# Optimization experiments

Measured on AMD Instinct MI355X. Metric: run time of the kernel, lower is better.

## Reference

```python
import jax, jax.numpy as jnp
import numpy as np

B, N, D, K, H, L = 4, 20000, 64, 256, 4, 2
F = 4 * D
DH = D // H
SCALE = DH ** -0.5
EPS = 1e-5


def _layernorm(x, g, b):
    m = jnp.mean(x, axis=-1, keepdims=True)
    v = jnp.mean(jnp.square(x - m), axis=-1, keepdims=True)
    return (x - m) / jnp.sqrt(v + EPS) * g + b


def setup_inputs() -> dict:
    key = jax.random.key(0)
    ks = jax.random.split(key, 12)
    s = 0.02
    return {
        'expr': jax.random.normal(ks[0], (B, N), jnp.float32),
        'emb': jax.random.normal(ks[1], (N, D), jnp.float32),
        'Wq': jax.random.normal(ks[2], (L, D, D), jnp.float32) * s,
        'Wk': jax.random.normal(ks[3], (L, D, D), jnp.float32) * s,
        'Wv': jax.random.normal(ks[4], (L, D, D), jnp.float32) * s,
        'projK': jax.random.normal(ks[5], (L, N, K), jnp.float32) * s,
        'projV': jax.random.normal(ks[6], (L, N, K), jnp.float32) * s,
        'Wo': jax.random.normal(ks[7], (L, D, D), jnp.float32) * s,
        'bo': jnp.zeros((L, D), jnp.float32),
        'g1': jnp.ones((L, D), jnp.float32),
        'be1': jnp.zeros((L, D), jnp.float32),
        'W1': jax.random.normal(ks[8], (L, D, F), jnp.float32) * s,
        'bf1': jnp.zeros((L, F), jnp.float32),
        'W2': jax.random.normal(ks[9], (L, F, D), jnp.float32) * s,
        'bf2': jnp.zeros((L, D), jnp.float32),
        'g2': jnp.ones((L, D), jnp.float32),
        'be2': jnp.zeros((L, D), jnp.float32),
    }


def _forward(expr, emb, Wq, Wk, Wv, projK, projV, Wo, bo, g1, be1, W1, bf1, W2, bf2, g2, be2):
    # gene_ids = arange(N) for every batch row -> embedding lookup is just the table
    x = emb[None, :, :] * expr[:, :, None]  # [B, N, D]
    for i in range(L):
        b = x.shape[0]
        # Linformer self-attention
        q = jnp.einsum('bnd,de->bne', x, Wq[i])                 # [B, N, D]
        k_low = jnp.einsum('bnd,nk->bkd', x, projK[i])          # [B, K, D]
        v_low = jnp.einsum('bnd,nk->bkd', x, projV[i])          # [B, K, D]
        k = jnp.einsum('bkd,de->bke', k_low, Wk[i])             # [B, K, D]
        v = jnp.einsum('bkd,de->bke', v_low, Wv[i])             # [B, K, D]
        qh = q.reshape(b, N, H, DH).transpose(0, 2, 1, 3)       # [B, H, N, DH]
        kh = k.reshape(b, K, H, DH).transpose(0, 2, 1, 3)       # [B, H, K, DH]
        vh = v.reshape(b, K, H, DH).transpose(0, 2, 1, 3)       # [B, H, K, DH]
        dots = jnp.einsum('bhnd,bhkd->bhnk', qh, kh) * SCALE    # [B, H, N, K]
        attn = jax.nn.softmax(dots, axis=-1)
        o = jnp.einsum('bhnk,bhkd->bhnd', attn, vh)             # [B, H, N, DH]
        o = o.transpose(0, 2, 1, 3).reshape(b, N, D)
        o = jnp.einsum('bnd,de->bne', o, Wo[i]) + bo[i]
        x = _layernorm(o + x, g1[i], be1[i])
        # FFN (exact GELU, matching torch nn.GELU default)
        h = jax.nn.gelu(jnp.einsum('bnd,df->bnf', x, W1[i]) + bf1[i], approximate=False)
        f = jnp.einsum('bnf,fd->bnd', h, W2[i]) + bf2[i]
        x = _layernorm(f + x, g2[i], be2[i])
    return x


def reference(expr, emb, Wq, Wk, Wv, projK, projV, Wo, bo, g1, be1, W1, bf1, W2, bf2, g2, be2):
    return _forward(expr, emb, Wq, Wk, Wv, projK, projV, Wo, bo, g1, be1, W1, bf1, W2, bf2, g2, be2)
```

## Files before the change

### kernel.cpp

```cpp
#include <hip/hip_runtime.h>

using u16 = unsigned short;
typedef __bf16 bf16x8 __attribute__((ext_vector_type(8)));
typedef u16    u16x8  __attribute__((ext_vector_type(8)));
typedef u16    u16x4  __attribute__((ext_vector_type(4)));
typedef float  f32x4  __attribute__((ext_vector_type(4)));
typedef float  f32x16 __attribute__((ext_vector_type(16)));
typedef unsigned uint4v __attribute__((ext_vector_type(4)));

#define DEV static __device__ __forceinline__

constexpr int NB = 4;
constexpr int NN = 20000;
constexpr int DD = 64;
constexpr int KK = 256;
constexpr int NT = 313;
constexpr int ROWS = NB * NN;

DEV float b2f(u16 u) { union { unsigned i; float f; } c; c.i = ((unsigned)u) << 16; return c.f; }
DEV u16 f2b(float f) {
  union { float f; unsigned i; } c; c.f = f;
  unsigned i = c.i + 0x7FFFu + ((c.i >> 16) & 1u);
  return (u16)(i >> 16);
}
DEV bf16x8 ldb8(const u16* p) { return *reinterpret_cast<const bf16x8*>(p); }
DEV f32x16 mfma32(bf16x8 a, bf16x8 b, f32x16 c) { return __builtin_amdgcn_mfma_f32_32x32x16_bf16(a, b, c, 0, 0, 0); }

DEV unsigned cvtpk(float lo, float hi) {
  unsigned r;
  asm("v_cvt_pk_bf16_f32 %0, %1, %2" : "=v"(r) : "v"(lo), "v"(hi));
  return r;
}
DEV void swap32(unsigned& a, unsigned& b) {
  auto r = __builtin_amdgcn_permlane32_swap((int)a, (int)b, false, false);
  a = (unsigned)r[0]; b = (unsigned)r[1];
}

__global__ __launch_bounds__(256) void k_pre(
    const float* __restrict__ expr, const float* __restrict__ emb,
    const float* __restrict__ Wq, const float* __restrict__ Wo,
    const float* __restrict__ W1, const float* __restrict__ W2,
    const float* __restrict__ projK, const float* __restrict__ projV,
    u16* __restrict__ wb, u16* __restrict__ pKT, u16* __restrict__ pVT,
    u16* __restrict__ xb, u16* __restrict__ ones) {
  __shared__ unsigned Lt[256][33];
  int bid = blockIdx.x;
  int t = threadIdx.x;
  if (bid < 1252) {
    int tile = bid % NT, z = bid / NT;
    int layer = z & 1, pv = z >> 1;
    const float* src = (pv ? projV : projK) + (size_t)layer * NN * KK;
    u16* dst = (pv ? pVT : pKT) + ((size_t)layer * NT + tile) * (256 * 64);
    int w = t >> 6, l = t & 63;
    int n0 = tile * 64;
    float4 v[16];
#pragma unroll
    for (int i = 0; i < 16; ++i) {
      int n = n0 + w * 16 + i;
      v[i] = (n < NN) ? reinterpret_cast<const float4*>(src)[(size_t)n * 64 + l]
                      : make_float4(0.f, 0.f, 0.f, 0.f);
    }
    int swz = ((l >> 1) & 7) << 2;
#pragma unroll
    for (int j = 0; j < 8; ++j) {
      int npx = (w * 8 + j) ^ swz;
#pragma unroll
      for (int c = 0; c < 4; ++c) {
        float a = (&v[2 * j].x)[c], b = (&v[2 * j + 1].x)[c];
        Lt[4 * l + c][npx] = cvtpk(a, b);
      }
    }
    __syncthreads();
    int q = t & 7, kk = t >> 3;
#pragma unroll
    for (int p = 0; p < 8; ++p) {
      int k = p * 32 + kk;
      int base = (q * 4) ^ (((k >> 3) & 7) << 2);
      uint4v o;
      o.x = Lt[k][base + 0]; o.y = Lt[k][base + 1];
      o.z = Lt[k][base + 2]; o.w = Lt[k][base + 3];
      *reinterpret_cast<uint4v*>(&dst[(size_t)k * 64 + q * 8]) = o;
    }
  } else if (bid < 3752) {
    int idx8 = ((bid - 1252) * 256 + t) * 8;
    int b = idx8 / (NN * DD);
    int rem = idx8 - b * (NN * DD);
    int n = rem >> 6, d = rem & 63;
    float4 e0 = *reinterpret_cast<const float4*>(&emb[(n << 6) + d]);
    float4 e1 = *reinterpret_cast<const float4*>(&emb[(n << 6) + d + 4]);
    float s = expr[b * NN + n];
    u16x8 o;
    o[0] = f2b(e0.x * s); o[1] = f2b(e0.y * s); o[2] = f2b(e0.z * s); o[3] = f2b(e0.w * s);
    o[4] = f2b(e1.x * s); o[5] = f2b(e1.y * s); o[6] = f2b(e1.z * s); o[7] = f2b(e1.w * s);
    *reinterpret_cast<u16x8*>(&xb[idx8]) = o;
  } else if (bid < 3816) {
    int b2 = bid - 3752;
    int bx = b2 & 7, m = (b2 >> 3) & 3, l = b2 >> 5;
    int slot = bx * 256 + t;
    u16x8 o;
    if (m <= 1) {
      if (slot >= 512) return;
      int s = slot >> 7, rem = slot & 127;
      int ct = rem >> 6, lane = rem & 63;
      int hi = lane >> 5, lo = lane & 31;
      const float* src = (m == 0 ? Wq : Wo) + l * 4096;
      u16* dst = wb + (m == 0 ? 0 : 8192) + l * 4096;
#pragma unroll
      for (int j = 0; j < 8; ++j) o[j] = f2b(src[(s * 16 + hi * 8 + j) * 64 + ct * 32 + lo]);
      *reinterpret_cast<u16x8*>(&dst[slot * 8]) = o;
    } else if (m == 2) {
      int ftile = slot >> 8, s = (slot >> 6) & 3, lane = slot & 63;
      int hi = lane >> 5, lo = lane & 31;
      const float* src = W1 + l * 16384;
      u16* dst = wb + 16384 + l * 16384;
#pragma unroll
      for (int j = 0; j < 8; ++j) o[j] = f2b(src[(s * 16 + hi * 8 + j) * 256 + ftile * 32 + lo]);
      *reinterpret_cast<u16x8*>(&dst[slot * 8]) = o;
    } else {
      int dtile = slot >> 10, s2 = (slot >> 6) & 15, lane = slot & 63;
      int hi = lane >> 5, lo = lane & 31;
      const float* src = W2 + l * 16384;
      u16* dst = wb + 49152 + l * 16384;
#pragma unroll
      for (int j = 0; j < 8; ++j) o[j] = f2b(src[(s2 * 16 + hi * 8 + j) * 64 + dtile * 32 + lo]);
      *reinterpret_cast<u16x8*>(&dst[slot * 8]) = o;
    }
  } else {
    ones[t] = 0x3F80;
  }
}

__global__ __launch_bounds__(256) void k_qxt(
    const u16* __restrict__ x, const u16* __restrict__ WB,
    u16* __restrict__ qb, u16* __restrict__ xT) {
  __shared__ u16 LX[64][67];
  int bid = blockIdx.x;
  int t = threadIdx.x;
  if (bid < 625) {
    int w = t >> 6, lane = t & 63;
    int lo = lane & 31, hi = lane >> 5;
    int unit = bid * 4 + w;
    bf16x8 wf[4][2];
#pragma unroll
    for (int s = 0; s < 4; ++s)
#pragma unroll
      for (int ct = 0; ct < 2; ++ct) wf[s][ct] = ldb8(&WB[((s * 2 + ct) * 64 + lane) * 8]);
    f32x16 acc[2] = {};
    int r0 = unit * 32;
#pragma unroll
    for (int s = 0; s < 4; ++s) {
      bf16x8 a = ldb8(&x[(size_t)(r0 + lo) * 64 + s * 16 + hi * 8]);
      acc[0] = mfma32(a, wf[s][0], acc[0]);
      acc[1] = mfma32(a, wf[s][1], acc[1]);
    }
#pragma unroll
    for (int reg = 0; reg < 16; ++reg) {
      int row = r0 + (reg & 3) + 8 * (reg >> 2) + 4 * hi;
      qb[(size_t)row * 64 + lo] = f2b(acc[0][reg]);
      qb[(size_t)row * 64 + 32 + lo] = f2b(acc[1][reg]);
    }
  } else {
    int v2 = bid - 625;
    int tile = v2 % NT, b = v2 / NT;
    const u16* xbp = x + (size_t)b * NN * 64;
    int n0 = tile * 64;
    int q = t & 7, rr = t >> 3;
    u16x8 h0 = {}, h1 = {};
    int na = n0 + rr, nb2 = n0 + 32 + rr;
    if (na < NN) h0 = *reinterpret_cast<const u16x8*>(&xbp[(size_t)na * 64 + q * 8]);
    if (nb2 < NN) h1 = *reinterpret_cast<const u16x8*>(&xbp[(size_t)nb2 * 64 + q * 8]);
#pragma unroll
    for (int c = 0; c < 8; ++c) {
      LX[q * 8 + c][rr] = h0[c];
      LX[q * 8 + c][32 + rr] = h1[c];
    }
    __syncthreads();
    u16* dstx = xT + ((size_t)b * NT + tile) * 4096;
#pragma unroll
    for (int p = 0; p < 2; ++p) {
      int d = p * 32 + rr;
      u16x8 o;
#pragma unroll
      for (int i = 0; i < 8; ++i) o[i] = LX[d][q * 8 + i];
      *reinterpret_cast<u16x8*>(&dstx[(size_t)d * 64 + q * 8]) = o;
    }
  }
}

__global__ __launch_bounds__(256) void k_proj(
    const u16* __restrict__ xT, const u16* __restrict__ pKT_l, const u16* __restrict__ pVT_l,
    float* __restrict__ part) {
  int c = blockIdx.x, b = blockIdx.y, proj = blockIdx.z;
  const u16* P = proj ? pVT_l : pKT_l;
  const u16* xtb = xT + (size_t)b * NT * 4096;
  int t = threadIdx.x, w = t >> 6, lane = t & 63;
  int lo = lane & 31, hi = lane >> 5;
  int d0 = (w & 1) * 32;
  int kbase = (w >> 1) * 128;
  int n0 = c * 512;
  int rem = NN - n0;
  int steps = (rem < 512 ? rem : 512) >> 4;
  int arow = (d0 + lo) * 64;
  f32x16 acc[4] = {};
  int s = 0;
  for (; s + 4 <= steps; s += 4) {
    int tile = (n0 + s * 16) >> 6;
    const u16* xa = xtb + (size_t)tile * 4096;
    const u16* Pa = P + (size_t)tile * 16384;
    bf16x8 a[4]; bf16x8 bv[4][4];
#pragma unroll
    for (int u = 0; u < 4; ++u) {
      int ni = u * 16 + hi * 8;
      a[u] = ldb8(&xa[arow + ni]);
#pragma unroll
      for (int g = 0; g < 4; ++g) bv[u][g] = ldb8(&Pa[(kbase + g * 32 + lo) * 64 + ni]);
    }
#pragma unroll
    for (int u = 0; u < 4; ++u)
#pragma unroll
      for (int g = 0; g < 4; ++g) acc[g] = mfma32(a[u], bv[u][g], acc[g]);
  }
  for (; s < steps; ++s) {
    int nb = n0 + s * 16;
    int tile = nb >> 6, ni = (nb & 63) + hi * 8;
    const u16* xa = xtb + (size_t)tile * 4096;
    const u16* Pa = P + (size_t)tile * 16384;
    bf16x8 a = ldb8(&xa[arow + ni]);
#pragma unroll
    for (int g = 0; g < 4; ++g) acc[g] = mfma32(a, ldb8(&Pa[(kbase + g * 32 + lo) * 64 + ni]), acc[g]);
  }
  float* dst = part + ((size_t)(proj * NB + b) * 40 + c) * (64 * 256);
#pragma unroll
  for (int g = 0; g < 4; ++g)
#pragma unroll
    for (int r = 0; r < 16; ++r) {
      int d = d0 + (r & 3) + 8 * (r >> 2) + 4 * hi;
      dst[d * 256 + kbase + g * 32 + lo] = acc[g][r];
    }
}

__global__ __launch_bounds__(256) void k_p2(
    const float* __restrict__ part, const float* __restrict__ Wk_l, const float* __restrict__ Wv_l,
    u16* __restrict__ kbuf, u16* __restrict__ vT) {
  int ks = blockIdx.x, b = blockIdx.y, proj = blockIdx.z;
  int k0 = ks * 8;
  const float* W = proj ? Wv_l : Wk_l;
  __shared__ float low[64][8];
  int t = threadIdx.x;
  const float* src = part + (size_t)(proj * NB + b) * 40 * (64 * 256);
#pragma unroll
  for (int i = 0; i < 2; ++i) {
    int idx = i * 256 + t;
    int e = idx >> 3, k = idx & 7;
    float s = 0.f;
    for (int cc = 0; cc < 40; ++cc) s += src[(size_t)cc * (64 * 256) + e * 256 + k0 + k];
    low[e][k] = s;
  }
  __syncthreads();
#pragma unroll
  for (int i = 0; i < 2; ++i) {
    int idx = i * 256 + t;
    int d = idx & 63, kk = idx >> 6;
    float a = 0.f;
#pragma unroll
    for (int e = 0; e < 64; ++e) a += low[e][kk] * W[e * 64 + d];
    if (proj == 0) {
      kbuf[((size_t)b * KK + k0 + kk) * 64 + d] = f2b(a * 0.3606737602222409f);
    } else {
      vT[((size_t)b * 64 + d) * KK + k0 + kk] = f2b(a);
    }
  }
}

__global__ __launch_bounds__(256) void k_attn(
    const u16* __restrict__ q, const u16* __restrict__ kbuf, const u16* __restrict__ vT,
    const u16* __restrict__ ones, u16* __restrict__ ao) {
  int t = threadIdx.x, h = t >> 6, lane = t & 63;
  int lo = lane & 31, hi = lane >> 5;
  int b = blockIdx.y;
  int n0 = blockIdx.x * 32;
  const u16* qb = q + (size_t)b * NN * 64;
  const u16* kb = kbuf + (size_t)b * KK * 64 + h * 16;
  const u16* vsrc = (lo < 16)
      ? vT + (size_t)b * 64 * KK + (size_t)(h * 16 + lo) * KK
      : ones;
  bf16x8 qf = ldb8(&qb[(size_t)(n0 + lo) * 64 + h * 16 + hi * 8]);
  f32x16 acc = {};
#pragma unroll
  for (int kt = 0; kt < 8; ++kt) {
    bf16x8 kf = ldb8(&kb[(size_t)(kt * 32 + lo) * 64 + hi * 8]);
    f32x16 z = {};
    f32x16 s = mfma32(kf, qf, z);
    float e[16];
#pragma unroll
    for (int r = 0; r < 16; ++r) e[r] = __builtin_amdgcn_exp2f(s[r]);
#pragma unroll
    for (int c = 0; c < 2; ++c) {
      unsigned Aw = cvtpk(e[c * 8 + 0], e[c * 8 + 1]);
      unsigned Bw = cvtpk(e[c * 8 + 2], e[c * 8 + 3]);
      unsigned Cw = cvtpk(e[c * 8 + 4], e[c * 8 + 5]);
      unsigned Dw = cvtpk(e[c * 8 + 6], e[c * 8 + 7]);
      swap32(Aw, Cw);
      swap32(Bw, Dw);
      uint4v pk; pk.x = Aw; pk.y = Bw; pk.z = Cw; pk.w = Dw;
      bf16x8 af = ldb8(&vsrc[kt * 32 + c * 16 + hi * 8]);
      acc = mfma32(af, __builtin_bit_cast(bf16x8, pk), acc);
    }
  }
  float inv = __builtin_amdgcn_rcpf(acc[8]);
  float o[8];
#pragma unroll
  for (int r = 0; r < 8; ++r) o[r] = acc[r] * inv;
  unsigned Aw = cvtpk(o[0], o[1]);
  unsigned Bw = cvtpk(o[2], o[3]);
  unsigned Cw = cvtpk(o[4], o[5]);
  unsigned Dw = cvtpk(o[6], o[7]);
  swap32(Aw, Cw);
  swap32(Bw, Dw);
  uint4v st; st.x = Aw; st.y = Bw; st.z = Cw; st.w = Dw;
  *reinterpret_cast<uint4v*>(&ao[(size_t)b * NN * 64 + (size_t)(n0 + lo) * 64 + h * 16 + hi * 8]) = st;
}

__global__ __launch_bounds__(256) void k_oln(
    const u16* __restrict__ A, const u16* __restrict__ WB,
    const float* __restrict__ bias, const u16* __restrict__ res,
    const float* __restrict__ g, const float* __restrict__ be, u16* __restrict__ out) {
  int t = threadIdx.x, w = t >> 6, lane = t & 63;
  int lo = lane & 31, hi = lane >> 5;
  int unit = blockIdx.x * 4 + w;
  bf16x8 wf[4][2];
#pragma unroll
  for (int s = 0; s < 4; ++s)
#pragma unroll
    for (int ct = 0; ct < 2; ++ct) wf[s][ct] = ldb8(&WB[((s * 2 + ct) * 64 + lane) * 8]);
  float bia[2], gg[2], bb[2];
#pragma unroll
  for (int ct = 0; ct < 2; ++ct) {
    bia[ct] = bias[ct * 32 + lo];
    gg[ct] = g[ct * 32 + lo];
    bb[ct] = be[ct * 32 + lo];
  }
  f32x16 acc[2] = {};
  int r0 = unit * 32;
#pragma unroll
  for (int s = 0; s < 4; ++s) {
    bf16x8 a = ldb8(&A[(size_t)(r0 + lo) * 64 + s * 16 + hi * 8]);
    acc[0] = mfma32(a, wf[s][0], acc[0]);
    acc[1] = mfma32(a, wf[s][1], acc[1]);
  }
#pragma unroll
  for (int reg = 0; reg < 16; ++reg) {
    int row = r0 + (reg & 3) + 8 * (reg >> 2) + 4 * hi;
    float a0 = acc[0][reg] + bia[0] + b2f(res[(size_t)row * 64 + lo]);
    float a1 = acc[1][reg] + bia[1] + b2f(res[(size_t)row * 64 + 32 + lo]);
    float su = a0 + a1, sq = a0 * a0 + a1 * a1;
#pragma unroll
    for (int m = 1; m <= 16; m <<= 1) { su += __shfl_xor(su, m); sq += __shfl_xor(sq, m); }
    float mean = su * (1.f / 64.f);
    float var = sq * (1.f / 64.f) - mean * mean;
    float rstd = rsqrtf(var + 1e-5f);
    out[(size_t)row * 64 + lo] = f2b((a0 - mean) * rstd * gg[0] + bb[0]);
    out[(size_t)row * 64 + 32 + lo] = f2b((a1 - mean) * rstd * gg[1] + bb[1]);
  }
}

__global__ __launch_bounds__(256) void k_ffn(
    const u16* __restrict__ A, const u16* __restrict__ W1T, const u16* __restrict__ W2T,
    const float* __restrict__ b1, const float* __restrict__ b2,
    const float* __restrict__ g, const float* __restrict__ be,
    u16* __restrict__ outb, float* __restrict__ outf) {
  int t = threadIdx.x, w = t >> 6, lane = t & 63;
  int lo = lane & 31, hi = lane >> 5;
  int unit = blockIdx.x * 4 + w;
  int r0 = unit * 32;
  bf16x8 xf[4];
#pragma unroll
  for (int s = 0; s < 4; ++s) xf[s] = ldb8(&A[(size_t)(r0 + lo) * 64 + s * 16 + hi * 8]);
  f32x16 oacc[2] = {};
#pragma unroll
  for (int ft = 0; ft < 8; ++ft) {
    f32x16 hacc = {};
#pragma unroll
    for (int s = 0; s < 4; ++s)
      hacc = mfma32(ldb8(&W1T[((ft * 4 + s) * 64 + lane) * 8]), xf[s], hacc);
    float4 bb[4];
#pragma unroll
    for (int g4 = 0; g4 < 4; ++g4)
      bb[g4] = *reinterpret_cast<const float4*>(&b1[ft * 32 + g4 * 8 + 4 * hi]);
    float e[16];
#pragma unroll
    for (int r = 0; r < 16; ++r) {
      float z = hacc[r] + bb[r >> 2][r & 3];
      e[r] = 0.5f * z * (1.f + erff(z * 0.7071067811865475f));
    }
#pragma unroll
    for (int c = 0; c < 2; ++c) {
      unsigned Aw = cvtpk(e[c * 8 + 0], e[c * 8 + 1]);
      unsigned Bw = cvtpk(e[c * 8 + 2], e[c * 8 + 3]);
      unsigned Cw = cvtpk(e[c * 8 + 4], e[c * 8 + 5]);
      unsigned Dw = cvtpk(e[c * 8 + 6], e[c * 8 + 7]);
      swap32(Aw, Cw);
      swap32(Bw, Dw);
      uint4v pk; pk.x = Aw; pk.y = Bw; pk.z = Cw; pk.w = Dw;
      bf16x8 pf = __builtin_bit_cast(bf16x8, pk);
#pragma unroll
      for (int dt = 0; dt < 2; ++dt)
        oacc[dt] = mfma32(ldb8(&W2T[((dt * 16 + ft * 2 + c) * 64 + lane) * 8]), pf, oacc[dt]);
    }
  }
  int n = r0 + lo;
  float su = 0.f, sq = 0.f;
#pragma unroll
  for (int dt = 0; dt < 2; ++dt) {
#pragma unroll
    for (int m4 = 0; m4 < 4; ++m4) {
      int d0 = dt * 32 + m4 * 8 + 4 * hi;
      u16x4 rv = *reinterpret_cast<const u16x4*>(&A[(size_t)n * 64 + d0]);
      float4 b2v = *reinterpret_cast<const float4*>(&b2[d0]);
#pragma unroll
      for (int j = 0; j < 4; ++j) {
        int r = m4 * 4 + j;
        float val = oacc[dt][r] + b2v[j] + b2f(rv[j]);
        oacc[dt][r] = val;
        su += val; sq += val * val;
      }
    }
  }
  su += __shfl_xor(su, 32);
  sq += __shfl_xor(sq, 32);
  float mean = su * (1.f / 64.f);
  float var = sq * (1.f / 64.f) - mean * mean;
  float rstd = rsqrtf(var + 1e-5f);
#pragma unroll
  for (int dt = 0; dt < 2; ++dt) {
#pragma unroll
    for (int m4 = 0; m4 < 4; ++m4) {
      int d0 = dt * 32 + m4 * 8 + 4 * hi;
      float4 gv = *reinterpret_cast<const float4*>(&g[d0]);
      float4 bv = *reinterpret_cast<const float4*>(&be[d0]);
      float q0 = (oacc[dt][m4 * 4 + 0] - mean) * rstd * gv.x + bv.x;
      float q1 = (oacc[dt][m4 * 4 + 1] - mean) * rstd * gv.y + bv.y;
      float q2 = (oacc[dt][m4 * 4 + 2] - mean) * rstd * gv.z + bv.z;
      float q3 = (oacc[dt][m4 * 4 + 3] - mean) * rstd * gv.w + bv.w;
      if (outb) {
        unsigned w0 = cvtpk(q0, q1), w1 = cvtpk(q2, q3);
        u16x4 st = __builtin_bit_cast(u16x4, make_uint2(w0, w1));
        *reinterpret_cast<u16x4*>(&outb[(size_t)n * 64 + d0]) = st;
      }
      if (outf) {
        *reinterpret_cast<float4*>(&outf[(size_t)n * 64 + d0]) = make_float4(q0, q1, q2, q3);
      }
    }
  }
}

extern "C" void kernel_launch(void* const* d_in, const int* in_sizes, int n_in,
                              void* d_out, int out_size, void* d_ws, size_t ws_size,
                              hipStream_t stream) {
  const float* expr = (const float*)d_in[0];
  const float* emb  = (const float*)d_in[1];
  const float* Wq   = (const float*)d_in[2];
  const float* Wk   = (const float*)d_in[3];
  const float* Wv   = (const float*)d_in[4];
  const float* projK = (const float*)d_in[5];
  const float* projV = (const float*)d_in[6];
  const float* Wo   = (const float*)d_in[7];
  const float* bo   = (const float*)d_in[8];
  const float* g1   = (const float*)d_in[9];
  const float* be1  = (const float*)d_in[10];
  const float* W1   = (const float*)d_in[11];
  const float* bf1  = (const float*)d_in[12];
  const float* W2   = (const float*)d_in[13];
  const float* bf2  = (const float*)d_in[14];
  const float* g2   = (const float*)d_in[15];
  const float* be2  = (const float*)d_in[16];
  float* out = (float*)d_out;
  char* ws = (char*)d_ws;

  u16* xb0 = (u16*)(ws + 0);
  u16* xb1 = (u16*)(ws + 10240000);
  u16* xb2 = (u16*)(ws + 20480000);
  u16* qb  = (u16*)(ws + 30720000);
  u16* aob = (u16*)(ws + 40960000);
  float* part = (float*)(ws + 51200000);
  u16* pKT = (u16*)(ws + 72171520);
  u16* pVT = (u16*)(ws + 92684288);
  u16* xTb = (u16*)(ws + 113197056);
  u16* kB  = (u16*)(ws + 123453440);
  u16* vTB = (u16*)(ws + 123584512);
  u16* wb  = (u16*)(ws + 123715584);
  u16* ones = (u16*)(ws + 123879424);

  k_pre<<<3817, 256, 0, stream>>>(expr, emb, Wq, Wo, W1, W2, projK, projV,
                                  wb, pKT, pVT, xb0, ones);

  const size_t PL = (size_t)NT * 256 * 64;
  const u16* xin = xb0;
  for (int l = 0; l < 2; ++l) {
    const u16* wbq = wb + l * 4096;
    const u16* wbo = wb + 8192 + l * 4096;
    const u16* wb1 = wb + 16384 + l * 16384;
    const u16* wb2 = wb + 49152 + l * 16384;
    k_qxt<<<1877, 256, 0, stream>>>(xin, wbq, qb, xTb);
    k_proj<<<dim3(40, NB, 2), 256, 0, stream>>>(xTb, pKT + (size_t)l * PL, pVT + (size_t)l * PL, part);
    k_p2<<<dim3(32, NB, 2), 256, 0, stream>>>(part, Wk + l * 4096, Wv + l * 4096, kB, vTB);
    k_attn<<<dim3(625, NB), 256, 0, stream>>>(qb, kB, vTB, ones, aob);
    k_oln<<<625, 256, 0, stream>>>(aob, wbo, bo + l * 64, xin, g1 + l * 64, be1 + l * 64, xb1);
    k_ffn<<<625, 256, 0, stream>>>(xb1, wb1, wb2, bf1 + l * 256, bf2 + l * 64,
                                   g2 + l * 64, be2 + l * 64,
                                   l == 0 ? xb2 : nullptr, l == 1 ? out : nullptr);
    xin = xb2;
  }
}
```

Baseline: 422.6 us.

## Split projection grid over K halves and move Q projection into reduce kernel

The k_proj grid is doubled by splitting the K dimension into two halves, so each wave keeps two accumulators instead of four and the inner loop is unrolled eight steps deep. This raises block count from 320 to 640 to fill more compute units. The Q projection moves out of the transpose kernel and into k_p2, so the small reduction blocks run alongside the Q GEMM blocks instead of launching a nearly empty grid. The cost is reloading the x tile once per K half in k_proj.

New measurement: 415.8 us. No clear change (-1.6%).

```diff
diff --git a/kernel.cpp b/kernel.cpp
--- a/kernel.cpp
+++ b/kernel.cpp
@@ -130,95 +130,68 @@
   }
 }
 
-__global__ __launch_bounds__(256) void k_qxt(
-    const u16* __restrict__ x, const u16* __restrict__ WB,
-    u16* __restrict__ qb, u16* __restrict__ xT) {
+__global__ __launch_bounds__(256) void k_xt(const u16* __restrict__ x, u16* __restrict__ xT) {
   __shared__ u16 LX[64][67];
-  int bid = blockIdx.x;
+  int tile = blockIdx.x, b = blockIdx.y;
   int t = threadIdx.x;
-  if (bid < 625) {
-    int w = t >> 6, lane = t & 63;
-    int lo = lane & 31, hi = lane >> 5;
-    int unit = bid * 4 + w;
-    bf16x8 wf[4][2];
-#pragma unroll
-    for (int s = 0; s < 4; ++s)
-#pragma unroll
-      for (int ct = 0; ct < 2; ++ct) wf[s][ct] = ldb8(&WB[((s * 2 + ct) * 64 + lane) * 8]);
-    f32x16 acc[2] = {};
-    int r0 = unit * 32;
-#pragma unroll
-    for (int s = 0; s < 4; ++s) {
-      bf16x8 a = ldb8(&x[(size_t)(r0 + lo) * 64 + s * 16 + hi * 8]);
-      acc[0] = mfma32(a, wf[s][0], acc[0]);
-      acc[1] = mfma32(a, wf[s][1], acc[1]);
-    }
-#pragma unroll
-    for (int reg = 0; reg < 16; ++reg) {
-      int row = r0 + (reg & 3) + 8 * (reg >> 2) + 4 * hi;
-      qb[(size_t)row * 64 + lo] = f2b(acc[0][reg]);
-      qb[(size_t)row * 64 + 32 + lo] = f2b(acc[1][reg]);
-    }
-  } else {
-    int v2 = bid - 625;
-    int tile = v2 % NT, b = v2 / NT;
-    const u16* xbp = x + (size_t)b * NN * 64;
-    int n0 = tile * 64;
-    int q = t & 7, rr = t >> 3;
-    u16x8 h0 = {}, h1 = {};
-    int na = n0 + rr, nb2 = n0 + 32 + rr;
-    if (na < NN) h0 = *reinterpret_cast<const u16x8*>(&xbp[(size_t)na * 64 + q * 8]);
-    if (nb2 < NN) h1 = *reinterpret_cast<const u16x8*>(&xbp[(size_t)nb2 * 64 + q * 8]);
-#pragma unroll
-    for (int c = 0; c < 8; ++c) {
-      LX[q * 8 + c][rr] = h0[c];
-      LX[q * 8 + c][32 + rr] = h1[c];
-    }
-    __syncthreads();
-    u16* dstx = xT + ((size_t)b * NT + tile) * 4096;
-#pragma unroll
-    for (int p = 0; p < 2; ++p) {
-      int d = p * 32 + rr;
-      u16x8 o;
-#pragma unroll
-      for (int i = 0; i < 8; ++i) o[i] = LX[d][q * 8 + i];
-      *reinterpret_cast<u16x8*>(&dstx[(size_t)d * 64 + q * 8]) = o;
-    }
+  const u16* xbp = x + (size_t)b * NN * 64;
+  int n0 = tile * 64;
+  int q = t & 7, rr = t >> 3;
+  u16x8 h0 = {}, h1 = {};
+  int na = n0 + rr, nb2 = n0 + 32 + rr;
+  if (na < NN) h0 = *reinterpret_cast<const u16x8*>(&xbp[(size_t)na * 64 + q * 8]);
+  if (nb2 < NN) h1 = *reinterpret_cast<const u16x8*>(&xbp[(size_t)nb2 * 64 + q * 8]);
+#pragma unroll
+  for (int c = 0; c < 8; ++c) {
+    LX[q * 8 + c][rr] = h0[c];
+    LX[q * 8 + c][32 + rr] = h1[c];
+  }
+  __syncthreads();
+  u16* dstx = xT + ((size_t)b * NT + tile) * 4096;
+#pragma unroll
+  for (int p = 0; p < 2; ++p) {
+    int d = p * 32 + rr;
+    u16x8 o;
+#pragma unroll
+    for (int i = 0; i < 8; ++i) o[i] = LX[d][q * 8 + i];
+    *reinterpret_cast<u16x8*>(&dstx[(size_t)d * 64 + q * 8]) = o;
   }
 }
 
 __global__ __launch_bounds__(256) void k_proj(
     const u16* __restrict__ xT, const u16* __restrict__ pKT_l, const u16* __restrict__ pVT_l,
     float* __restrict__ part) {
-  int c = blockIdx.x, b = blockIdx.y, proj = blockIdx.z;
+  int c = blockIdx.x, b = blockIdx.y;
+  int proj = blockIdx.z & 1, ks = blockIdx.z >> 1;
   const u16* P = proj ? pVT_l : pKT_l;
   const u16* xtb = xT + (size_t)b * NT * 4096;
   int t = threadIdx.x, w = t >> 6, lane = t & 63;
   int lo = lane & 31, hi = lane >> 5;
   int d0 = (w & 1) * 32;
-  int kbase = (w >> 1) * 128;
+  int kbase = ks * 128 + (w >> 1) * 64;
   int n0 = c * 512;
   int rem = NN - n0;
   int steps = (rem < 512 ? rem : 512) >> 4;
   int arow = (d0 + lo) * 64;
-  f32x16 acc[4] = {};
+  f32x16 acc[2] = {};
   int s = 0;
-  for (; s + 4 <= steps; s += 4) {
-    int tile = (n0 + s * 16) >> 6;
-    const u16* xa = xtb + (size_t)tile * 4096;
-    const u16* Pa = P + (size_t)tile * 16384;
-    bf16x8 a[4]; bf16x8 bv[4][4];
-#pragma unroll
-    for (int u = 0; u < 4; ++u) {
-      int ni = u * 16 + hi * 8;
+  for (; s + 8 <= steps; s += 8) {
+    bf16x8 a[8]; bf16x8 bv[8][2];
+#pragma unroll
+    for (int u = 0; u < 8; ++u) {
+      int nb = n0 + (s + u) * 16;
+      int tile = nb >> 6, ni = (nb & 63) + hi * 8;
+      const u16* xa = xtb + (size_t)tile * 4096;
+      const u16* Pa = P + (size_t)tile * 16384;
       a[u] = ldb8(&xa[arow + ni]);
-#pragma unroll
-      for (int g = 0; g < 4; ++g) bv[u][g] = ldb8(&Pa[(kbase + g * 32 + lo) * 64 + ni]);
-    }
-#pragma unroll
-    for (int u = 0; u < 4; ++u)
-#pragma unroll
-      for (int g = 0; g < 4; ++g) acc[g] = mfma32(a[u], bv[u][g], acc[g]);
+      bv[u][0] = ldb8(&Pa[(kbase + lo) * 64 + ni]);
+      bv[u][1] = ldb8(&Pa[(kbase + 32 + lo) * 64 + ni]);
+    }
+#pragma unroll
+    for (int u = 0; u < 8; ++u) {
+      acc[0] = mfma32(a[u], bv[u][0], acc[0]);
+      acc[1] = mfma32(a[u], bv[u][1], acc[1]);
+    }
   }
   for (; s < steps; ++s) {
     int nb = n0 + s * 16;
@@ -226,12 +199,12 @@
     const u16* xa = xtb + (size_t)tile * 4096;
     const u16* Pa = P + (size_t)tile * 16384;
     bf16x8 a = ldb8(&xa[arow + ni]);
-#pragma unroll
-    for (int g = 0; g < 4; ++g) acc[g] = mfma32(a, ldb8(&Pa[(kbase + g * 32 + lo) * 64 + ni]), acc[g]);
+    acc[0] = mfma32(a, ldb8(&Pa[(kbase + lo) * 64 + ni]), acc[0]);
+    acc[1] = mfma32(a, ldb8(&Pa[(kbase + 32 + lo) * 64 + ni]), acc[1]);
   }
   float* dst = part + ((size_t)(proj * NB + b) * 40 + c) * (64 * 256);
 #pragma unroll
-  for (int g = 0; g < 4; ++g)
+  for (int g = 0; g < 2; ++g)
 #pragma unroll
     for (int r = 0; r < 16; ++r) {
       int d = d0 + (r & 3) + 8 * (r >> 2) + 4 * hi;
@@ -241,33 +214,60 @@
 
 __global__ __launch_bounds__(256) void k_p2(
     const float* __restrict__ part, const float* __restrict__ Wk_l, const float* __restrict__ Wv_l,
-    u16* __restrict__ kbuf, u16* __restrict__ vT) {
-  int ks = blockIdx.x, b = blockIdx.y, proj = blockIdx.z;
-  int k0 = ks * 8;
-  const float* W = proj ? Wv_l : Wk_l;
+    u16* __restrict__ kbuf, u16* __restrict__ vT,
+    const u16* __restrict__ x, const u16* __restrict__ WQB, u16* __restrict__ qb) {
   __shared__ float low[64][8];
+  int bid = blockIdx.x;
   int t = threadIdx.x;
-  const float* src = part + (size_t)(proj * NB + b) * 40 * (64 * 256);
-#pragma unroll
-  for (int i = 0; i < 2; ++i) {
-    int idx = i * 256 + t;
-    int e = idx >> 3, k = idx & 7;
-    float s = 0.f;
-    for (int cc = 0; cc < 40; ++cc) s += src[(size_t)cc * (64 * 256) + e * 256 + k0 + k];
-    low[e][k] = s;
-  }
-  __syncthreads();
-#pragma unroll
-  for (int i = 0; i < 2; ++i) {
-    int idx = i * 256 + t;
-    int d = idx & 63, kk = idx >> 6;
-    float a = 0.f;
-#pragma unroll
-    for (int e = 0; e < 64; ++e) a += low[e][kk] * W[e * 64 + d];
-    if (proj == 0) {
-      kbuf[((size_t)b * KK + k0 + kk) * 64 + d] = f2b(a * 0.3606737602222409f);
-    } else {
-      vT[((size_t)b * 64 + d) * KK + k0 + kk] = f2b(a);
+  if (bid < 256) {
+    int ks = bid & 31, b = (bid >> 5) & 3, proj = bid >> 7;
+    int k0 = ks * 8;
+    const float* W = proj ? Wv_l : Wk_l;
+    const float* src = part + (size_t)(proj * NB + b) * 40 * (64 * 256);
+#pragma unroll
+    for (int i = 0; i < 2; ++i) {
+      int idx = i * 256 + t;
+      int e = idx >> 3, k = idx & 7;
+      float s = 0.f;
+      for (int cc = 0; cc < 40; ++cc) s += src[(size_t)cc * (64 * 256) + e * 256 + k0 + k];
+      low[e][k] = s;
+    }
+    __syncthreads();
+#pragma unroll
+    for (int i = 0; i < 2; ++i) {
+      int idx = i * 256 + t;
+      int d = idx & 63, kk = idx >> 6;
+      float a = 0.f;
+#pragma unroll
+      for (int e = 0; e < 64; ++e) a += low[e][kk] * W[e * 64 + d];
+      if (proj == 0) {
+        kbuf[((size_t)b * KK + k0 + kk) * 64 + d] = f2b(a * 0.3606737602222409f);
+      } else {
+        vT[((size_t)b * 64 + d) * KK + k0 + kk] = f2b(a);
+      }
+    }
+  } else {
+    int w = t >> 6, lane = t & 63;
+    int lo = lane & 31, hi = lane >> 5;
+    int unit = (bid - 256) * 4 + w;
+    bf16x8 wf[4][2];
+#pragma unroll
+    for (int s = 0; s < 4; ++s)
+#pragma unroll
+      for (int ct = 0; ct < 2; ++ct) wf[s][ct] = ldb8(&WQB[((s * 2 + ct) * 64 + lane) * 8]);
+    f32x16 acc[2] = {};
+    int r0 = unit * 32;
+#pragma unroll
+    for (int s = 0; s < 4; ++s) {
+      bf16x8 a = ldb8(&x[(size_t)(r0 + lo) * 64 + s * 16 + hi * 8]);
+      acc[0] = mfma32(a, wf[s][0], acc[0]);
+      acc[1] = mfma32(a, wf[s][1], acc[1]);
+    }
+#pragma unroll
+    for (int reg = 0; reg < 16; ++reg) {
+      int row = r0 + (reg & 3) + 8 * (reg >> 2) + 4 * hi;
+      qb[(size_t)row * 64 + lo] = f2b(acc[0][reg]);
+      qb[(size_t)row * 64 + 32 + lo] = f2b(acc[1][reg]);
     }
   }
 }
@@ -501,9 +501,10 @@
     const u16* wbo = wb + 8192 + l * 4096;
     const u16* wb1 = wb + 16384 + l * 16384;
     const u16* wb2 = wb + 49152 + l * 16384;
-    k_qxt<<<1877, 256, 0, stream>>>(xin, wbq, qb, xTb);
-    k_proj<<<dim3(40, NB, 2), 256, 0, stream>>>(xTb, pKT + (size_t)l * PL, pVT + (size_t)l * PL, part);
-    k_p2<<<dim3(32, NB, 2), 256, 0, stream>>>(part, Wk + l * 4096, Wv + l * 4096, kB, vTB);
+    k_xt<<<dim3(NT, NB), 256, 0, stream>>>(xin, xTb);
+    k_proj<<<dim3(40, NB, 4), 256, 0, stream>>>(xTb, pKT + (size_t)l * PL, pVT + (size_t)l * PL, part);
+    k_p2<<<881, 256, 0, stream>>>(part, Wk + l * 4096, Wv + l * 4096, kB, vTB,
+                                  xin, wbq, qb);
     k_attn<<<dim3(625, NB), 256, 0, stream>>>(qb, kB, vTB, ones, aob);
     k_oln<<<625, 256, 0, stream>>>(aob, wbo, bo + l * 64, xin, g1 + l * 64, be1 + l * 64, xb1);
     k_ffn<<<625, 256, 0, stream>>>(xb1, wb1, wb2, bf1 + l * 256, bf2 + l * 64,
```
